# Kernel optimization log

Hardware: AMD Instinct MI355X
Metric: run time of the kernel (lower is better)

Reference implementation:

```python
import jax, jax.numpy as jnp
import numpy as np

KSIZE, STRIDES, D_NEURON, DK, DV, NH, DACT, FINAL_DIM = 4, 2, 128, 128, 256, 8, 8, 256
N = KSIZE * KSIZE          # 16 neurons per window
DKH = DK // NH             # 16 == N (required by broadcast in original code)
DVH = DV // NH             # 32


def setup_inputs() -> dict:
    key = jax.random.key(0)
    ks = jax.random.split(key, 12)
    B, H, W, C = 32, 64, 64, 256
    def dense(kw, kb, fan_in, fan_out):
        w = jax.random.normal(kw, (fan_in, fan_out), jnp.float32) / np.sqrt(fan_in)
        b = jnp.zeros((fan_out,), jnp.float32)
        return w, b
    inps = jax.random.normal(ks[0], (B, H, W, C), jnp.float32)
    neuron_emb = jax.random.normal(ks[1], (KSIZE, KSIZE, D_NEURON), jnp.float32) / np.sqrt(D_NEURON)
    wkq_w, wkq_b = dense(ks[2], ks[3], D_NEURON, 2 * DK)
    wv_w, wv_b = dense(ks[4], ks[5], C, DV)
    wgactq_w, wgactq_b = dense(ks[6], ks[7], D_NEURON, DACT)
    wgactk_w, wgactk_b = dense(ks[8], ks[9], C, DACT)
    wf_w, wf_b = dense(ks[10], ks[11], DV, FINAL_DIM)
    return dict(inps=inps, neuron_emb=neuron_emb, wkq_w=wkq_w, wkq_b=wkq_b,
                wv_w=wv_w, wv_b=wv_b, wgactq_w=wgactq_w, wgactq_b=wgactq_b,
                wgactk_w=wgactk_w, wgactk_b=wgactk_b, wf_w=wf_w, wf_b=wf_b)


def _forward(inps, neuron_emb, wkq_w, wkq_b, wv_w, wv_b,
             wgactq_w, wgactq_b, wgactk_w, wgactk_b, wf_w, wf_b):
    B, H, W, C = inps.shape
    # ---- neural structures (tiny, per-head n x n softmax) ----
    kq = neuron_emb @ wkq_w + wkq_b                      # (k,k,2dk)
    k_part, q_part = jnp.split(kq, 2, axis=-1)           # each (k,k,dk)
    flat = lambda t: t.reshape(N, NH, DKH).transpose(1, 0, 2)   # (Nh,n,dkh)
    fk, fq = flat(k_part), flat(q_part)
    # broadcast add requires dkh == n: logits[h,i,j] = fq[h,i,j] + fk[h,j,i]
    logits = fq + fk.transpose(0, 2, 1)                  # (Nh,n,n)
    structures = jax.nn.softmax(logits, axis=-1)
    s0 = structures[:, 0, :]                             # (Nh,n) row 0 per head
    # ---- activation amounts (dacth == 1, i.e. dact == Nh) ----
    actk = inps @ wgactk_w + wgactk_b                    # (B,H,W,Nh)
    actq = (neuron_emb @ wgactq_w + wgactq_b).reshape(N, NH)   # (n,Nh)
    qv = actq[N - 2]                                     # slice [-2:-1] -> (Nh,)
    g = jax.nn.relu(qv[None, None, None, :] + actk)      # (B,H,W,Nh)
    denom = jnp.sum(g, axis=(1, 2), keepdims=True)       # (B,1,1,Nh)
    act = (float(H * W) / (denom + 1e-6)) * g            # (B,H,W,Nh)
    # ---- values, gated per head ----
    v = inps @ wv_w + wv_b                               # (B,H,W,dv)
    v = (v.reshape(B, H, W, NH, DVH) * act[..., None]).reshape(B, H, W, DV)
    # ---- SAME-padded im2col patches (TF extract_patches ordering kh,kw,c) ----
    nH, nW = -(-H // STRIDES), -(-W // STRIDES)
    pad_h = max((nH - 1) * STRIDES + KSIZE - H, 0)
    pad_w = max((nW - 1) * STRIDES + KSIZE - W, 0)
    vp = jnp.pad(v, ((0, 0), (pad_h // 2, pad_h - pad_h // 2),
                     (pad_w // 2, pad_w - pad_w // 2), (0, 0)))
    hi = (nH - 1) * STRIDES + 1
    wi = (nW - 1) * STRIDES + 1
    patches = jnp.stack([vp[:, i:i + hi:STRIDES, j:j + wi:STRIDES, :]
                         for i in range(KSIZE) for j in range(KSIZE)],
                        axis=3)                           # (B,nH,nW,n,dv)
    p = patches.reshape(B, nH, nW, N, NH, DVH)
    # weighted reduce over window positions with structure row 0
    out = jnp.einsum('hn,bxynhd->bxyhd', s0, p).reshape(B, nH, nW, DV)
    return out @ wf_w + wf_b                             # (B,nH,nW,final_dim)


def reference(inps, neuron_emb, wkq_w, wkq_b, wv_w, wv_b,
              wgactq_w, wgactq_b, wgactk_w, wgactk_b, wf_w, wf_b):
    return _forward(inps, neuron_emb, wkq_w, wkq_b, wv_w, wv_b,
                    wgactq_w, wgactq_b, wgactk_w, wgactk_b, wf_w, wf_b)
```

## Files before the change

### kernel.cpp

```cpp
#include <hip/hip_runtime.h>
#include <hip/hip_bf16.h>

#define B_    32
#define H_    64
#define W_    64
#define C_    256
#define NH_   8
#define N_    16
#define PIX_  (B_*H_*W_)
#define OUTPIX_ (B_*32*32)

typedef __hip_bfloat16 bf16;
typedef __attribute__((ext_vector_type(8))) short bf16x8;
typedef __attribute__((ext_vector_type(4))) float f32x4;

__device__ __forceinline__ float bf2f(unsigned short u) {
  union { unsigned int i; float f; } v; v.i = ((unsigned int)u) << 16; return v.f;
}
__device__ __forceinline__ unsigned pk2(float a, float b) {
  union { __hip_bfloat162 h2; unsigned u; } c;
  c.h2 = __float22bfloat162_rn(make_float2(a, b));
  return c.u;
}

__global__ __launch_bounds__(256) void k1_setup(
    const float* __restrict__ emb, const float* __restrict__ wkq_w,
    const float* __restrict__ wkq_b, const float* __restrict__ wgq_w,
    const float* __restrict__ wgq_b,
    float* __restrict__ s0, float* __restrict__ qv) {
  __shared__ float lq[128];
  __shared__ float lk[16][8];
  int t = threadIdx.x;
  if (t < 128) {
    float acc = wkq_b[128 + t];
    for (int e = 0; e < 128; ++e) acc += emb[e] * wkq_w[e * 256 + 128 + t];
    lq[t] = acc;
  } else {
    int idx = t - 128; int j = idx >> 3, h = idx & 7;
    float acc = wkq_b[h * 16];
    for (int e = 0; e < 128; ++e) acc += emb[j * 128 + e] * wkq_w[e * 256 + h * 16];
    lk[j][h] = acc;
  }
  __syncthreads();
  if (t < 8) {
    float l[16]; float m = -1e30f;
    for (int j = 0; j < 16; ++j) { l[j] = lq[t * 16 + j] + lk[j][t]; m = fmaxf(m, l[j]); }
    float s = 0.f;
    for (int j = 0; j < 16; ++j) { l[j] = expf(l[j] - m); s += l[j]; }
    float inv = 1.f / s;
    for (int j = 0; j < 16; ++j) s0[t * 16 + j] = l[j] * inv;
    float acc = wgq_b[t];
    for (int e = 0; e < 128; ++e) acc += emb[14 * 128 + e] * wgq_w[e * 8 + t];
    qv[t] = acc;
  }
}

__global__ __launch_bounds__(256) void prep(
    const float* __restrict__ wv, const float* __restrict__ wf,
    const float* __restrict__ wgk,
    bf16* __restrict__ wvT, bf16* __restrict__ wfT, bf16* __restrict__ wgkT) {
  int bid = blockIdx.x, t = threadIdx.x;
  if (bid < 32) {
    __shared__ unsigned short tile[64][72];
    const float* src = (bid < 16) ? wv : wf;
    bf16* dst = (bid < 16) ? wvT : wfT;
    int tb = bid & 15, tr = tb >> 2, tc = tb & 3;
#pragma unroll
    for (int it = 0; it < 16; ++it) {
      int idx = it * 256 + t, row = idx >> 6, col = idx & 63;
      bf16 h = __float2bfloat16(src[(tr * 64 + row) * 256 + tc * 64 + col]);
      tile[row][col] = *(unsigned short*)&h;
    }
    __syncthreads();
#pragma unroll
    for (int it = 0; it < 16; ++it) {
      int idx = it * 256 + t, row = idx >> 6, col = idx & 63;
      dst[(tc * 64 + row) * 256 + (tr * 64 + col)] = *(bf16*)&tile[col][row];
    }
  } else {
    __shared__ float g[2048];
#pragma unroll
    for (int it = 0; it < 8; ++it) g[it * 256 + t] = wgk[it * 256 + t];
    __syncthreads();
#pragma unroll
    for (int it = 0; it < 16; ++it) {
      int idx = it * 256 + t, a = idx >> 8, k = idx & 255;
      float v = (a < 8) ? g[k * 8 + a] : 0.f;
      wgkT[a * 256 + k] = __float2bfloat16(v);
    }
  }
}

#define KA_TILES 4
__global__ __launch_bounds__(512, 4) void kA(
    const float* __restrict__ inps, const bf16* __restrict__ wvT,
    const bf16* __restrict__ wgkT, const float* __restrict__ wv_b,
    const float* __restrict__ wgk_b, const float* __restrict__ qv,
    bf16* __restrict__ vraw, float* __restrict__ gbuf,
    float* __restrict__ denom) {
  __shared__ __align__(16) unsigned short ldsA[2][64][136];
  __shared__ float sden[8];
  __shared__ float qvb_s[8];
  int t = threadIdx.x;
  int bid = blockIdx.x;
  const long px_base = (long)bid * (KA_TILES * 64);
  if (t < 8) { sden[t] = 0.f; qvb_s[t] = qv[t] + wgk_b[t]; }

  int wave = t >> 6, lane = t & 63;
  int mw = wave >> 2, nw = wave & 3;
  int m0 = mw * 32, n0 = nw * 64;
  int lm = lane & 15, q = lane >> 4;
  bool gatew = (nw == 0);
  const bf16* brow = wvT + (n0 + lm) * 256;
  const bf16* grow = wgkT + lm * 256;

  int sr = t >> 5, sc4 = t & 31;
  const float* sbase = inps + px_base * 256 + sr * 256 + sc4 * 4;
  float4 st[4];

#define LOADST(ph_)                                                          \
  {                                                                          \
    const float* s_ = sbase + ((ph_) >> 1) * (64 * 256) + ((ph_) & 1) * 128; \
    _Pragma("unroll")                                                        \
    for (int it = 0; it < 4; ++it)                                           \
      st[it] = *(const float4*)(s_ + it * 16 * 256);                         \
  }
#define WRITEST(bufi_)                                                       \
  {                                                                          \
    _Pragma("unroll")                                                        \
    for (int it = 0; it < 4; ++it)                                           \
      *(uint2*)&ldsA[bufi_][it * 16 + sr][sc4 * 4] =                         \
          make_uint2(pk2(st[it].x, st[it].y), pk2(st[it].z, st[it].w));      \
  }

  LOADST(0);
  WRITEST(0);
  LOADST(1);
  __syncthreads();

  f32x4 acc[2][4], accg[2];
  float gsum = 0.f;

#pragma unroll 2
  for (int ph = 0; ph < 2 * KA_TILES; ++ph) {
    const int cur = ph & 1;
    if (cur == 0) {
#pragma unroll
      for (int mf = 0; mf < 2; ++mf) {
        accg[mf] = (f32x4){0.f, 0.f, 0.f, 0.f};
#pragma unroll
        for (int nf = 0; nf < 4; ++nf) acc[mf][nf] = (f32x4){0.f, 0.f, 0.f, 0.f};
      }
    }
    const unsigned short* arow0 = &ldsA[cur][m0 + lm][0];
    const unsigned short* arow1 = &ldsA[cur][m0 + 16 + lm][0];
#pragma unroll
    for (int ksl = 0; ksl < 4; ++ksl) {
      int kof = ksl * 32 + q * 8;
      bf16x8 a0 = *(const bf16x8*)(arow0 + kof);
      bf16x8 a1 = *(const bf16x8*)(arow1 + kof);
      int gk = cur * 128 + kof;
      bf16x8 b0 = *(const bf16x8*)(brow + gk);
      bf16x8 b1 = *(const bf16x8*)(brow + 4096 + gk);
      bf16x8 b2 = *(const bf16x8*)(brow + 8192 + gk);
      bf16x8 b3 = *(const bf16x8*)(brow + 12288 + gk);
      acc[0][0] = __builtin_amdgcn_mfma_f32_16x16x32_bf16(a0, b0, acc[0][0], 0, 0, 0);
      acc[1][0] = __builtin_amdgcn_mfma_f32_16x16x32_bf16(a1, b0, acc[1][0], 0, 0, 0);
      acc[0][1] = __builtin_amdgcn_mfma_f32_16x16x32_bf16(a0, b1, acc[0][1], 0, 0, 0);
      acc[1][1] = __builtin_amdgcn_mfma_f32_16x16x32_bf16(a1, b1, acc[1][1], 0, 0, 0);
      acc[0][2] = __builtin_amdgcn_mfma_f32_16x16x32_bf16(a0, b2, acc[0][2], 0, 0, 0);
      acc[1][2] = __builtin_amdgcn_mfma_f32_16x16x32_bf16(a1, b2, acc[1][2], 0, 0, 0);
      acc[0][3] = __builtin_amdgcn_mfma_f32_16x16x32_bf16(a0, b3, acc[0][3], 0, 0, 0);
      acc[1][3] = __builtin_amdgcn_mfma_f32_16x16x32_bf16(a1, b3, acc[1][3], 0, 0, 0);
      if (gatew) {
        bf16x8 bg = *(const bf16x8*)(grow + gk);
        accg[0] = __builtin_amdgcn_mfma_f32_16x16x32_bf16(a0, bg, accg[0], 0, 0, 0);
        accg[1] = __builtin_amdgcn_mfma_f32_16x16x32_bf16(a1, bg, accg[1], 0, 0, 0);
      }
    }

    if (cur == 1) {
      long pix0 = px_base + (ph >> 1) * 64;
#pragma unroll
      for (int nf = 0; nf < 4; ++nf) {
        int col = n0 + nf * 16 + lm;
        float wb = wv_b[col];
#pragma unroll
        for (int mf = 0; mf < 2; ++mf) {
#pragma unroll
          for (int r = 0; r < 4; ++r) {
            int rl = m0 + mf * 16 + q * 4 + r;
            vraw[(pix0 + rl) * 256 + col] = __float2bfloat16(acc[mf][nf][r] + wb);
          }
        }
      }
      if (gatew && lm < 8) {
#pragma unroll
        for (int mf = 0; mf < 2; ++mf) {
#pragma unroll
          for (int r = 0; r < 4; ++r) {
            int rl = m0 + mf * 16 + q * 4 + r;
            float gg = fmaxf(qvb_s[lm] + accg[mf][r], 0.f);
            gbuf[(pix0 + rl) * 8 + lm] = gg;
            gsum += gg;
          }
        }
      }
    }

    if (ph < 2 * KA_TILES - 1) {
      WRITEST(cur ^ 1);
      if (ph < 2 * KA_TILES - 2) LOADST(ph + 2);
    }
    __syncthreads();
  }

  if (gatew) {
    gsum += __shfl_xor(gsum, 16, 64);
    gsum += __shfl_xor(gsum, 32, 64);
    if (lane < 8) atomicAdd(&sden[lane], gsum);
  }
  __syncthreads();
  if (t < 8) atomicAdd(&denom[(bid >> 4) * 8 + t], sden[t]);
#undef LOADST
#undef WRITEST
}

__global__ __launch_bounds__(256) void kB(
    const bf16* __restrict__ vraw, const float* __restrict__ s0,
    const float* __restrict__ gbuf, const float* __restrict__ denom,
    const bf16* __restrict__ wfT, const float* __restrict__ wf_b,
    float* __restrict__ out) {
  __shared__ float scfsh[4][64][8];
  __shared__ __align__(16) unsigned short opsh[32][264];
  int t = threadIdx.x;
  int bx = blockIdx.x, b = bx >> 5, x = bx & 31;

  {
    int i = t >> 6, c = t & 63;
    int r = 2 * x + i - 1;
    if (r >= 0 && r < 64) {
      long p = (long)b * 4096 + r * 64 + c;
#pragma unroll
      for (int a = 0; a < 8; ++a)
        scfsh[i][c][a] = 4096.0f / (denom[b * 8 + a] + 1e-6f) * gbuf[p * 8 + a];
    } else {
#pragma unroll
      for (int a = 0; a < 8; ++a) scfsh[i][c][a] = 0.f;
    }
  }
  __syncthreads();

  int c2 = t & 127, yg = t >> 7;
  int h = c2 >> 4;
  float s0r[16];
#pragma unroll
  for (int n = 0; n < 16; ++n) s0r[n] = s0[h * 16 + n];
  const bf16* vsb = vraw + (long)b * (4096 * 256);
  for (int yi = 0; yi < 16; ++yi) {
    int y = yi * 2 + yg;
    float p0 = 0.f, p1 = 0.f;
#pragma unroll
    for (int i = 0; i < 4; ++i) {
      int r = 2 * x + i - 1;
      if (r < 0 || r >= 64) continue;
      const bf16* rowp = vsb + (long)r * 64 * 256 + 2 * c2;
#pragma unroll
      for (int j = 0; j < 4; ++j) {
        int c = 2 * y + j - 1;
        if (c < 0 || c >= 64) continue;
        float coef = s0r[i * 4 + j] * scfsh[i][c][h];
        unsigned u = *(const unsigned*)(rowp + (long)c * 256);
        p0 += coef * bf2f((unsigned short)(u & 0xffff));
        p1 += coef * bf2f((unsigned short)(u >> 16));
      }
    }
    *(unsigned*)&opsh[y][2 * c2] = pk2(p0, p1);
  }
  __syncthreads();

  int wave = t >> 6, lane = t & 63;
  int n0 = wave * 64;
  int lm = lane & 15, q = lane >> 4;
  f32x4 acc[2][4];
#pragma unroll
  for (int mf = 0; mf < 2; ++mf)
#pragma unroll
    for (int nf = 0; nf < 4; ++nf) acc[mf][nf] = (f32x4){0.f, 0.f, 0.f, 0.f};
  const bf16* brow = wfT + (n0 + lm) * 256;
#pragma unroll
  for (int ks = 0; ks < 8; ++ks) {
    int kof = ks * 32 + q * 8;
    bf16x8 a0 = *(const bf16x8*)(&opsh[lm][kof]);
    bf16x8 a1 = *(const bf16x8*)(&opsh[16 + lm][kof]);
#pragma unroll
    for (int nf = 0; nf < 4; ++nf) {
      bf16x8 bb = *(const bf16x8*)(brow + nf * 4096 + kof);
      acc[0][nf] = __builtin_amdgcn_mfma_f32_16x16x32_bf16(a0, bb, acc[0][nf], 0, 0, 0);
      acc[1][nf] = __builtin_amdgcn_mfma_f32_16x16x32_bf16(a1, bb, acc[1][nf], 0, 0, 0);
    }
  }
  long out0 = (long)bx * 32 * 256;
#pragma unroll
  for (int nf = 0; nf < 4; ++nf) {
    int col = n0 + nf * 16 + lm;
    float wb = wf_b[col];
#pragma unroll
    for (int mf = 0; mf < 2; ++mf) {
#pragma unroll
      for (int r = 0; r < 4; ++r) {
        int row = mf * 16 + q * 4 + r;
        out[out0 + row * 256 + col] = acc[mf][nf][r] + wb;
      }
    }
  }
}

extern "C" void kernel_launch(void* const* d_in, const int* in_sizes, int n_in,
                              void* d_out, int out_size, void* d_ws, size_t ws_size,
                              hipStream_t stream) {
  const float* inps  = (const float*)d_in[0];
  const float* emb   = (const float*)d_in[1];
  const float* wkq_w = (const float*)d_in[2];
  const float* wkq_b = (const float*)d_in[3];
  const float* wv_w  = (const float*)d_in[4];
  const float* wv_b  = (const float*)d_in[5];
  const float* wgq_w = (const float*)d_in[6];
  const float* wgq_b = (const float*)d_in[7];
  const float* wgk_w = (const float*)d_in[8];
  const float* wgk_b = (const float*)d_in[9];
  const float* wf_w  = (const float*)d_in[10];
  const float* wf_b  = (const float*)d_in[11];

  float* wsf   = (float*)d_ws;
  float* s0f   = wsf;
  float* qvf   = wsf + 128;
  float* denom = wsf + 256;
  float* gbuf  = wsf + 1024;
  bf16*  wvT   = (bf16*)(wsf + 1049600);
  bf16*  wfT   = (bf16*)(wsf + 1082368);
  bf16*  wgkT  = (bf16*)(wsf + 1115136);
  bf16*  vraw  = (bf16*)(wsf + 1117184);
  float* outp  = (float*)d_out;

  hipMemsetAsync((void*)denom, 0, 1024, stream);
  k1_setup<<<1, 256, 0, stream>>>(emb, wkq_w, wkq_b, wgq_w, wgq_b, s0f, qvf);
  prep<<<33, 256, 0, stream>>>(wv_w, wf_w, wgk_w, wvT, wfT, wgkT);
  kA<<<PIX_ / (KA_TILES * 64), 512, 0, stream>>>(inps, wvT, wgkT, wv_b, wgk_b, qvf,
                                                 vraw, gbuf, denom);
  kB<<<OUTPIX_ / 32, 256, 0, stream>>>(vraw, s0f, gbuf, denom, wfT, wf_b, outp);
}
```

Baseline: 406.4 us.

## Stage fp32 input tiles into LDS with async global_load_lds and XOR swizzle

Result: slower. 417.3 us (+2.7%).

```diff
diff --git a/kernel.cpp b/kernel.cpp
--- a/kernel.cpp
+++ b/kernel.cpp
@@ -21,6 +21,17 @@
   union { __hip_bfloat162 h2; unsigned u; } c;
   c.h2 = __float22bfloat162_rn(make_float2(a, b));
   return c.u;
+}
+__device__ __forceinline__ bf16x8 cvt8(float4 lo, float4 hi) {
+  union { bf16x8 v; unsigned u[4]; } r;
+  r.u[0] = pk2(lo.x, lo.y); r.u[1] = pk2(lo.z, lo.w);
+  r.u[2] = pk2(hi.x, hi.y); r.u[3] = pk2(hi.z, hi.w);
+  return r.v;
+}
+__device__ __forceinline__ void async_copy16(void* lds, const void* g) {
+  __builtin_amdgcn_global_load_lds(
+      (const __attribute__((address_space(1))) unsigned int*)g,
+      (__attribute__((address_space(3))) unsigned int*)lds, 16, 0, 0);
 }
 
 __global__ __launch_bounds__(256) void k1_setup(
@@ -98,7 +109,7 @@
     const float* __restrict__ wgk_b, const float* __restrict__ qv,
     bf16* __restrict__ vraw, float* __restrict__ gbuf,
     float* __restrict__ denom) {
-  __shared__ __align__(16) unsigned short ldsA[2][64][136];
+  __shared__ __align__(16) float ldsA[2][64][128];
   __shared__ float sden[8];
   __shared__ float qvb_s[8];
   int t = threadIdx.x;
@@ -114,29 +125,28 @@
   const bf16* brow = wvT + (n0 + lm) * 256;
   const bf16* grow = wgkT + lm * 256;
 
-  int sr = t >> 5, sc4 = t & 31;
-  const float* sbase = inps + px_base * 256 + sr * 256 + sc4 * 4;
-  float4 st[4];
-
-#define LOADST(ph_)                                                          \
-  {                                                                          \
-    const float* s_ = sbase + ((ph_) >> 1) * (64 * 256) + ((ph_) & 1) * 128; \
-    _Pragma("unroll")                                                        \
-    for (int it = 0; it < 4; ++it)                                           \
-      st[it] = *(const float4*)(s_ + it * 16 * 256);                         \
-  }
-#define WRITEST(bufi_)                                                       \
-  {                                                                          \
-    _Pragma("unroll")                                                        \
-    for (int it = 0; it < 4; ++it)                                           \
-      *(uint2*)&ldsA[bufi_][it * 16 + sr][sc4 * 4] =                         \
-          make_uint2(pk2(st[it].x, st[it].y), pk2(st[it].z, st[it].w));      \
-  }
-
-  LOADST(0);
-  WRITEST(0);
-  LOADST(1);
-  __syncthreads();
+  const int s_u = lane & 31;
+  const int s_rh = lane >> 5;
+#define STAGE(ph_, bufi_)                                                     \
+  {                                                                           \
+    const float* gb_ =                                                        \
+        inps + (px_base + ((ph_) >> 1) * 64) * 256 + ((ph_) & 1) * 128;       \
+    _Pragma("unroll")                                                         \
+    for (int i_ = 0; i_ < 4; ++i_) {                                          \
+      int r_ = 8 * wave + 2 * i_ + s_rh;                                      \
+      const float* g_ = gb_ + r_ * 256 + ((s_u ^ (r_ & 7)) << 2);             \
+      async_copy16(&ldsA[bufi_][8 * wave + 2 * i_][0], g_);                   \
+    }                                                                         \
+  }
+
+  STAGE(0, 0);
+  __syncthreads();
+
+  const float4* pA0 = (const float4*)&ldsA[0][0][0];
+  const float4* pA1 = (const float4*)&ldsA[1][0][0];
+  const int rx = (m0 + lm) & 7;
+  const int i0 = (m0 + lm) * 32;
+  const int i1 = (m0 + 16 + lm) * 32;
 
   f32x4 acc[2][4], accg[2];
   float gsum = 0.f;
@@ -144,6 +154,7 @@
 #pragma unroll 2
   for (int ph = 0; ph < 2 * KA_TILES; ++ph) {
     const int cur = ph & 1;
+    if (ph < 2 * KA_TILES - 1) STAGE(ph + 1, cur ^ 1);
     if (cur == 0) {
 #pragma unroll
       for (int mf = 0; mf < 2; ++mf) {
@@ -152,14 +163,15 @@
         for (int nf = 0; nf < 4; ++nf) acc[mf][nf] = (f32x4){0.f, 0.f, 0.f, 0.f};
       }
     }
-    const unsigned short* arow0 = &ldsA[cur][m0 + lm][0];
-    const unsigned short* arow1 = &ldsA[cur][m0 + 16 + lm][0];
+    const float4* pA = cur ? pA1 : pA0;
 #pragma unroll
     for (int ksl = 0; ksl < 4; ++ksl) {
-      int kof = ksl * 32 + q * 8;
-      bf16x8 a0 = *(const bf16x8*)(arow0 + kof);
-      bf16x8 a1 = *(const bf16x8*)(arow1 + kof);
-      int gk = cur * 128 + kof;
+      int ulo = (ksl * 8 + q * 2) ^ rx;
+      float4 a0lo = pA[i0 + ulo], a0hi = pA[i0 + (ulo ^ 1)];
+      float4 a1lo = pA[i1 + ulo], a1hi = pA[i1 + (ulo ^ 1)];
+      bf16x8 a0 = cvt8(a0lo, a0hi);
+      bf16x8 a1 = cvt8(a1lo, a1hi);
+      int gk = cur * 128 + ksl * 32 + q * 8;
       bf16x8 b0 = *(const bf16x8*)(brow + gk);
       bf16x8 b1 = *(const bf16x8*)(brow + 4096 + gk);
       bf16x8 b2 = *(const bf16x8*)(brow + 8192 + gk);
@@ -207,11 +219,6 @@
         }
       }
     }
-
-    if (ph < 2 * KA_TILES - 1) {
-      WRITEST(cur ^ 1);
-      if (ph < 2 * KA_TILES - 2) LOADST(ph + 2);
-    }
     __syncthreads();
   }
 
@@ -222,8 +229,7 @@
   }
   __syncthreads();
   if (t < 8) atomicAdd(&denom[(bid >> 4) * 8 + t], sden[t]);
-#undef LOADST
-#undef WRITEST
+#undef STAGE
 }
 
 __global__ __launch_bounds__(256) void kB(
```
